# Optimization experiments

Hardware: AMD Instinct MI355X
Metric: run time of the kernel (lower is better)

The kernel has to match this reference:

```python
import jax, jax.numpy as jnp
import numpy as np


def setup_inputs() -> dict:
    key = jax.random.key(0)
    B, E, K = 1024, 1024, 64
    k0, k1, k2, k3, k4, k5 = jax.random.split(key, 6)
    s = 1.0 / np.sqrt(E)  # PyTorch GRU init bound
    c = jax.random.normal(k0, (B, E), dtype=jnp.float32)
    x = jax.random.normal(k1, (B, E, K), dtype=jnp.float32)
    W_ih = jax.random.uniform(k2, (3 * E, E), minval=-s, maxval=s, dtype=jnp.float32)
    W_hh = jax.random.uniform(k3, (3 * E, E), minval=-s, maxval=s, dtype=jnp.float32)
    b_ih = jax.random.uniform(k4, (3 * E,), minval=-s, maxval=s, dtype=jnp.float32)
    b_hh = jax.random.uniform(k5, (3 * E,), minval=-s, maxval=s, dtype=jnp.float32)
    return {"c": c, "x": x, "W_ih": W_ih, "W_hh": W_hh, "b_ih": b_ih, "b_hh": b_hh, "K": K}


def reference(c, x, W_ih, W_hh, b_ih, b_hh, K):
    # c: (B, E) initial hidden state; x: (B, E, T) teacher-forcing sequence.
    # Inputs actually consumed by the GRU: zeros at step 0, then x columns
    # [T-K .. T-2] at steps 1..K-1 (the torch slice at the last step is empty
    # and never used).
    B, E = c.shape
    T = x.shape[2]
    x_t = jnp.transpose(x, (2, 0, 1))  # (T, B, E)
    xs = jnp.concatenate(
        [jnp.zeros((1, B, E), dtype=x.dtype), x_t[T - K : T - 1]], axis=0
    )  # (K, B, E)

    def step(h, xk):
        gi = xk @ W_ih.T + b_ih  # (B, 3E)
        gh = h @ W_hh.T + b_hh   # (B, 3E)
        i_r, i_z, i_n = jnp.split(gi, 3, axis=-1)
        h_r, h_z, h_n = jnp.split(gh, 3, axis=-1)
        r = jax.nn.sigmoid(i_r + h_r)
        z = jax.nn.sigmoid(i_z + h_z)
        n = jnp.tanh(i_n + r * h_n)
        h_new = (1.0 - z) * n + z * h
        return h_new, h_new

    _, ys = jax.lax.scan(step, c, xs)  # ys: (K, B, E)
    y = jnp.transpose(ys, (1, 0, 2))   # (B, K, E) == torch.cat(y_out, dim=1)
    return jnp.transpose(y, (0, 2, 1))  # teacher-forcing transpose -> (B, E, K)
```

## Files before the change

### kernel.cpp

```cpp
#include <hip/hip_runtime.h>
#include <hip/hip_bf16.h>
#include <math.h>

typedef __bf16 bf16x8 __attribute__((ext_vector_type(8)));
typedef float f32x4 __attribute__((ext_vector_type(4)));
typedef unsigned short u16x8 __attribute__((ext_vector_type(8)));

#define VMW(N) asm volatile("s_waitcnt vmcnt(" #N ")" ::: "memory")
#define LGKM0  asm volatile("s_waitcnt lgkmcnt(0)" ::: "memory")
#define CFENCE asm volatile("" ::: "memory")

__device__ inline unsigned short f2b(float f) {
  union { float f; unsigned u; } v; v.f = f;
  unsigned u = v.u;
  return (unsigned short)((u + 0x7fffu + ((u >> 16) & 1u)) >> 16);
}
__device__ inline float b2f(unsigned short s) {
  union { unsigned u; float f; } v; v.u = ((unsigned)s) << 16;
  return v.f;
}
__device__ inline float sigm(float x) { return 1.f / (1.f + __expf(-x)); }
__device__ inline float tanh_f(float x) {
  float e = __expf(2.f * x);
  return 1.f - 2.f / (e + 1.f);
}
__device__ inline void gll16(const unsigned short* g, unsigned short* l) {
  __builtin_amdgcn_global_load_lds(
      (const __attribute__((address_space(1))) void*)g,
      (__attribute__((address_space(3))) void*)l, 16, 0, 0);
}
__device__ inline void gll16u(const unsigned short* g, unsigned short* l) {
  __builtin_amdgcn_global_load_lds(
      (const __attribute__((address_space(1))) void*)g,
      (__attribute__((address_space(3))) void*)l, 16, 0, 17);
}
__device__ inline void as64(unsigned short* p, unsigned long long v) {
  __hip_atomic_store((unsigned long long*)p, v, __ATOMIC_RELAXED,
                     __HIP_MEMORY_SCOPE_AGENT);
}

__global__ __launch_bounds__(256) void prep_kernel(
    const float* __restrict__ Wih, const float* __restrict__ Whh,
    const float* __restrict__ c, unsigned short* __restrict__ Wihb,
    unsigned short* __restrict__ Whhb, unsigned short* __restrict__ hbf,
    float* __restrict__ h32, long nW, long nH)
{
  long stride = (long)gridDim.x * blockDim.x;
  long t0 = (long)blockIdx.x * blockDim.x + threadIdx.x;
  for (long i = t0; i < nW; i += stride) {
    Wihb[i] = f2b(Wih[i]);
    Whhb[i] = f2b(Whh[i]);
  }
  for (long i = t0; i < nH; i += stride) {
    float v = c[i];
    h32[i] = v;
    hbf[i] = f2b(v);
  }
}

__global__ __launch_bounds__(256) void reorder_kernel(
    const unsigned short* __restrict__ Wihb, const unsigned short* __restrict__ Whhb,
    const float* __restrict__ bih, const float* __restrict__ bhh,
    unsigned short* __restrict__ Wihp, unsigned short* __restrict__ Whhp,
    float* __restrict__ bihp, float* __restrict__ bhhp, int E)
{
  int N3 = 3 * E;
  long total = (long)N3 * E;
  long stride = (long)gridDim.x * blockDim.x;
  long t0 = (long)blockIdx.x * blockDim.x + threadIdx.x;
  for (long i = t0; i < total; i += stride) {
    int rp = (int)(i / E);
    int col = (int)(i - (long)rp * E);
    int g6 = rp / 192, rem = rp - g6 * 192;
    int g = rem >> 6, elo = rem & 63;
    long src = ((long)g * E + g6 * 64 + elo) * E + col;
    Wihp[i] = Wihb[src];
    Whhp[i] = Whhb[src];
  }
  for (long i = t0; i < N3; i += stride) {
    int rp = (int)i;
    int g6 = rp / 192, rem = rp - g6 * 192;
    int g = rem >> 6, elo = rem & 63;
    bihp[i] = bih[(long)g * E + g6 * 64 + elo];
    bhhp[i] = bhh[(long)g * E + g6 * 64 + elo];
  }
}

__global__ __launch_bounds__(256) void transpose_x(
    const float* __restrict__ x, unsigned short* __restrict__ XS,
    int B, int E, int K)
{
  __shared__ float T[64][65];
  int e0 = blockIdx.x * 64;
  int b = blockIdx.y;
  int t = threadIdx.x;
  const float* xb = x + ((long)b * E + e0) * K;
#pragma unroll
  for (int i = 0; i < 4; ++i) {
    int cidx = i * 256 + t;
    int e = cidx >> 4;
    int f4 = cidx & 15;
    float4 v = *(const float4*)(xb + (long)e * K + f4 * 4);
    T[e][f4 * 4 + 0] = v.x;
    T[e][f4 * 4 + 1] = v.y;
    T[e][f4 * 4 + 2] = v.z;
    T[e][f4 * 4 + 3] = v.w;
  }
  __syncthreads();
#pragma unroll
  for (int i = 0; i < 16; ++i) {
    int cidx = i * 256 + t;
    int k = cidx >> 6;
    int e = cidx & 63;
    if (k < K - 1)
      XS[((long)(k + 1) * B + b) * E + e0 + e] = f2b(T[e][k]);
  }
}

__global__ __launch_bounds__(512, 1)
void gemm256(const unsigned short* __restrict__ A,
             const unsigned short* __restrict__ Bw,
             const float* __restrict__ bias,
             unsigned short* __restrict__ Cb,
             int M, int N, int K)
{
  __shared__ __align__(16) unsigned short sm[3 * 24576];

  int nwg = gridDim.x * gridDim.y;
  int wg = blockIdx.y * gridDim.x + blockIdx.x;
  if ((nwg & 7) == 0) { int ch = nwg >> 3; wg = (wg & 7) * ch + (wg >> 3); }
  int tx = wg % gridDim.x;
  int ty = wg / gridDim.x;

  const int tid = threadIdx.x;
  const int lane = tid & 63;
  const int wave = tid >> 6;
  const int wm = wave >> 2;
  const int wn = wave & 3;
  const int q = lane >> 4;
  const int l15 = lane & 15;

  const long a_base = (long)ty * 128 * K;
  const long b_base = (long)tx * 256 * K;

  long a_src[2]; int a_dst[2];
#pragma unroll
  for (int i = 0; i < 2; ++i) {
    int c = i * 512 + tid;
    int row = c >> 3;
    int g8 = (c & 7) ^ (row & 7);
    a_src[i] = a_base + (long)row * K + g8 * 8;
    a_dst[i] = c * 8;
  }
  long b_src[4]; int b_dst[4];
#pragma unroll
  for (int i = 0; i < 4; ++i) {
    int c = i * 512 + tid;
    int row = c >> 3;
    int g8 = (c & 7) ^ (row & 7);
    b_src[i] = b_base + (long)row * K + g8 * 8;
    b_dst[i] = c * 8;
  }

  int a_ro[4], b_ro[4];
#pragma unroll
  for (int mi = 0; mi < 4; ++mi) {
    int lr = wm * 64 + mi * 16 + l15;
    a_ro[mi] = lr * 64;
  }
#pragma unroll
  for (int ni = 0; ni < 4; ++ni) {
    int col = wn * 64 + ni * 16 + l15;
    b_ro[ni] = col * 64;
  }

  f32x4 acc[4][4] = {};

  const int NT = K >> 6;
#pragma unroll
  for (int t = 0; t < 2; ++t) {
    unsigned short* As = sm + t * 24576;
    unsigned short* Bs = As + 8192;
#pragma unroll
    for (int i = 0; i < 2; ++i) gll16(A + a_src[i] + t * 64, As + a_dst[i]);
#pragma unroll
    for (int i = 0; i < 4; ++i) gll16(Bw + b_src[i] + t * 64, Bs + b_dst[i]);
  }

  for (int kt = 0; kt < NT; ++kt) {
    if (kt >= NT - 2) VMW(0); else VMW(6);
    __builtin_amdgcn_s_barrier();
    CFENCE;
    const unsigned short* As = sm + (kt % 3) * 24576;
    const unsigned short* Bs = As + 8192;
    unsigned short* As2 = sm + ((kt + 2) % 3) * 24576;
    unsigned short* Bs2 = As2 + 8192;
    const bool st = (kt + 2 < NT);
    const int ko = (kt + 2) * 64;

    if (st) {
      gll16(A + a_src[0] + ko, As2 + a_dst[0]);
      gll16(A + a_src[1] + ko, As2 + a_dst[1]);
      gll16(Bw + b_src[0] + ko, Bs2 + b_dst[0]);
    }
    {
      const int c8 = q;
      bf16x8 af[4], bf_[4];
#pragma unroll
      for (int mi = 0; mi < 4; ++mi) {
        int lr = wm * 64 + mi * 16 + l15;
        af[mi] = *(const bf16x8*)&As[a_ro[mi] + ((c8 ^ (lr & 7)) << 3)];
      }
#pragma unroll
      for (int ni = 0; ni < 4; ++ni) {
        int col = wn * 64 + ni * 16 + l15;
        bf_[ni] = *(const bf16x8*)&Bs[b_ro[ni] + ((c8 ^ (col & 7)) << 3)];
      }
      __builtin_amdgcn_s_setprio(1);
#pragma unroll
      for (int mi = 0; mi < 4; ++mi)
#pragma unroll
        for (int ni = 0; ni < 4; ++ni)
          acc[mi][ni] = __builtin_amdgcn_mfma_f32_16x16x32_bf16(
              af[mi], bf_[ni], acc[mi][ni], 0, 0, 0);
      __builtin_amdgcn_s_setprio(0);
    }
    LGKM0;
    __builtin_amdgcn_s_barrier();
    CFENCE;
    if (st) {
      gll16(Bw + b_src[1] + ko, Bs2 + b_dst[1]);
      gll16(Bw + b_src[2] + ko, Bs2 + b_dst[2]);
      gll16(Bw + b_src[3] + ko, Bs2 + b_dst[3]);
    }
    {
      const int c8 = 4 + q;
      bf16x8 af[4], bf_[4];
#pragma unroll
      for (int mi = 0; mi < 4; ++mi) {
        int lr = wm * 64 + mi * 16 + l15;
        af[mi] = *(const bf16x8*)&As[a_ro[mi] + ((c8 ^ (lr & 7)) << 3)];
      }
#pragma unroll
      for (int ni = 0; ni < 4; ++ni) {
        int col = wn * 64 + ni * 16 + l15;
        bf_[ni] = *(const bf16x8*)&Bs[b_ro[ni] + ((c8 ^ (col & 7)) << 3)];
      }
      __builtin_amdgcn_s_setprio(1);
#pragma unroll
      for (int mi = 0; mi < 4; ++mi)
#pragma unroll
        for (int ni = 0; ni < 4; ++ni)
          acc[mi][ni] = __builtin_amdgcn_mfma_f32_16x16x32_bf16(
              af[mi], bf_[ni], acc[mi][ni], 0, 0, 0);
      __builtin_amdgcn_s_setprio(0);
    }
    LGKM0;
  }

  long crow0 = (long)ty * 128 + wm * 64;
  long ccol0 = (long)tx * 256 + wn * 64;
#pragma unroll
  for (int mi = 0; mi < 4; ++mi) {
#pragma unroll
    for (int ni = 0; ni < 4; ++ni) {
      long col = ccol0 + ni * 16 + l15;
      float bv = bias[col];
#pragma unroll
      for (int j = 0; j < 4; ++j) {
        long row = crow0 + mi * 16 + (q << 2) + j;
        Cb[row * N + col] = f2b(acc[mi][ni][j] + bv);
      }
    }
  }
}

#define BM 128
#define BN 128
#define BKS 64

template<int OUTBF>
__global__ __launch_bounds__(256)
void gemm_bt(const unsigned short* __restrict__ A,
             const unsigned short* __restrict__ Bw,
             const float* __restrict__ bias,
             float* __restrict__ Cf, unsigned short* __restrict__ Cb,
             int M, int N, int K)
{
  __shared__ __align__(16) unsigned short As[BM * BKS];
  __shared__ __align__(16) unsigned short Bs[BN * BKS];

  int nwg = gridDim.x * gridDim.y;
  int wg = blockIdx.y * gridDim.x + blockIdx.x;
  if ((nwg & 7) == 0) { int ch = nwg >> 3; wg = (wg & 7) * ch + (wg >> 3); }
  int tx = wg % gridDim.x;
  int ty = wg / gridDim.x;

  const int tid = threadIdx.x;
  const int lane = tid & 63;
  const int wave = tid >> 6;
  const int wr = wave >> 1, wc = wave & 1;

  f32x4 acc[4][4] = {};

  const long a_base = (long)ty * BM * K;
  const long b_base = (long)tx * BN * K;

  for (int kt = 0; kt < K; kt += BKS) {
    __syncthreads();
#pragma unroll
    for (int i = 0; i < 4; ++i) {
      int c = i * 256 + tid;
      int row = c >> 3, sc = c & 7;
      int gcol8 = sc ^ (row & 7);
      const unsigned short* ga = A + a_base + (long)row * K + kt + gcol8 * 8;
      const unsigned short* gb = Bw + b_base + (long)row * K + kt + gcol8 * 8;
      int cbase = (i * 256 + wave * 64) * 8;
      gll16(ga, &As[cbase]);
      gll16(gb, &Bs[cbase]);
    }
    __syncthreads();
#pragma unroll
    for (int kk = 0; kk < BKS; kk += 32) {
      int kidx = kk + ((lane >> 4) << 3);
      int c8 = kidx >> 3;
      bf16x8 af[4], bfv[4];
#pragma unroll
      for (int m = 0; m < 4; ++m) {
        int row = wr * 64 + m * 16 + (lane & 15);
        af[m] = *(const bf16x8*)&As[row * BKS + ((c8 ^ (row & 7)) << 3)];
      }
#pragma unroll
      for (int n = 0; n < 4; ++n) {
        int col = wc * 64 + n * 16 + (lane & 15);
        bfv[n] = *(const bf16x8*)&Bs[col * BKS + ((c8 ^ (col & 7)) << 3)];
      }
#pragma unroll
      for (int m = 0; m < 4; ++m)
#pragma unroll
        for (int n = 0; n < 4; ++n)
          acc[m][n] = __builtin_amdgcn_mfma_f32_16x16x32_bf16(
              af[m], bfv[n], acc[m][n], 0, 0, 0);
    }
  }

  long crow0 = (long)ty * BM + wr * 64;
  long ccol0 = (long)tx * BN + wc * 64;
#pragma unroll
  for (int m = 0; m < 4; ++m) {
#pragma unroll
    for (int n = 0; n < 4; ++n) {
      long col = ccol0 + n * 16 + (lane & 15);
      float bv = bias[col];
#pragma unroll
      for (int j = 0; j < 4; ++j) {
        long row = crow0 + m * 16 + ((lane >> 4) << 2) + j;
        float v = acc[m][n][j] + bv;
        if (OUTBF) Cb[row * N + col] = f2b(v);
        else       Cf[row * N + col] = v;
      }
    }
  }
}

__global__ __launch_bounds__(512, 1)
void gru_rec4(const unsigned short* __restrict__ GI,
              const unsigned short* __restrict__ Whp,
              const float* __restrict__ bhp,
              const unsigned short* __restrict__ h0,
              unsigned short* __restrict__ hbuf0,
              unsigned short* __restrict__ hbuf1,
              unsigned short* __restrict__ Y,
              unsigned int* __restrict__ bar,
              int B, int E, int K, int net)
{
  __shared__ __align__(16) unsigned char smem[156672];
  unsigned short* Ah  = (unsigned short*)smem;
  unsigned short* Bss = (unsigned short*)(smem + 49152);
  unsigned short* GIs = (unsigned short*)(smem + 122880);
  unsigned short* Ys  = (unsigned short*)(smem + 147456);
  float* Red = (float*)smem;

  const int N3 = 3 * E;
  const int e6 = blockIdx.x;
  const int bt = blockIdx.y;
  const int b0 = bt << 6;
  const int ec0 = e6 * 192;
  const int ecol0 = e6 << 6;
  const int tid = threadIdx.x;
  const int lane = tid & 63;
  const int w = tid >> 6;
  const int ew = w >> 1;
  const int kw = w & 1;
  const int q = lane >> 4;
  const int l15 = lane & 15;
  const int el = (ew << 4) + l15;
  const int c8 = (kw << 2) + q;
  const int axo = (c8 ^ (l15 & 7)) << 3;
  const int bxo = (c8 ^ (el & 7)) << 3;

  const int arow = tid >> 3;
  const int ag8 = (tid & 7) ^ (arow & 7);
  const long a_goff = (long)(b0 + arow) * E + ag8 * 8;
  const int a_dst = tid * 8;
  long b_goff[3]; int b_dst[3];
#pragma unroll
  for (int i = 0; i < 3; ++i) {
    int c = i * 512 + tid;
    int row = c >> 3;
    int g8 = (c & 7) ^ (row & 7);
    b_goff[i] = (long)(ec0 + row) * E + g8 * 8;
    b_dst[i] = c * 8;
  }
  long gi_off[3]; int gi_dst[3];
#pragma unroll
  for (int i = 0; i < 3; ++i) {
    int c = i * 512 + tid;
    int row = c / 24, cc = c - row * 24;
    gi_off[i] = (long)(b0 + row) * N3 + ec0 + cc * 8;
    gi_dst[i] = c * 8;
  }

  const float bh0 = bhp[ec0 + el];
  const float bh1 = bhp[ec0 + 64 + el];
  const float bh2 = bhp[ec0 + 128 + el];

  if (kw == 0) {
#pragma unroll
    for (int m = 0; m < 4; ++m)
#pragma unroll
      for (int j = 0; j < 4; ++j) {
        int row = m * 16 + q * 4 + j;
        Ys[row * 72 + el] = h0[(long)(b0 + row) * E + ecol0 + el];
      }
  }
  __syncthreads();

  for (int k = 0; k < K; ++k) {
    const unsigned short* hprev = (k & 1) ? hbuf1 : hbuf0;
    unsigned short* hnext = (k & 1) ? hbuf0 : hbuf1;
    const unsigned short* GIk = GI + (long)k * B * N3;

#pragma unroll
    for (int i = 0; i < 3; ++i) gll16(GIk + gi_off[i], GIs + gi_dst[i]);
#pragma unroll
    for (int t = 0; t < 5; ++t)
      gll16u(hprev + a_goff + t * 64, Ah + t * 4096 + a_dst);
#pragma unroll
    for (int t = 0; t < 2; ++t)
#pragma unroll
      for (int i = 0; i < 3; ++i)
        gll16(Whp + b_goff[i] + t * 64, Bss + t * 12288 + b_dst[i]);

    f32x4 acc[4][3];
#pragma unroll
    for (int m = 0; m < 4; ++m)
#pragma unroll
      for (int g = 0; g < 3; ++g)
        acc[m][g] = (f32x4){0.f, 0.f, 0.f, 0.f};

#pragma unroll
    for (int kt = 0; kt < 16; ++kt) {
      if (kt == 0)       VMW(3);
      else if (kt == 1)  VMW(4);
      else if (kt <= 11) VMW(5);
      else if (kt == 12) VMW(4);
      else if (kt == 15) VMW(0);
      else               VMW(3);
      LGKM0;
      __builtin_amdgcn_s_barrier();
      CFENCE;

      if (kt + 2 < 16) {
#pragma unroll
        for (int i = 0; i < 3; ++i)
          gll16(Whp + b_goff[i] + (kt + 2) * 64,
                Bss + ((kt + 2) % 3) * 12288 + b_dst[i]);
      }
      if (kt + 5 < 16)
        gll16u(hprev + a_goff + (kt + 5) * 64,
               Ah + ((kt + 5) % 6) * 4096 + a_dst);

      const unsigned short* Ab = Ah + (kt % 6) * 4096;
      const unsigned short* Bb = Bss + (kt % 3) * 12288;
      bf16x8 af[4], bfg[3];
#pragma unroll
      for (int m = 0; m < 4; ++m)
        af[m] = *(const bf16x8*)&Ab[(m * 16 + l15) * 64 + axo];
#pragma unroll
      for (int g = 0; g < 3; ++g)
        bfg[g] = *(const bf16x8*)&Bb[(g * 64 + el) * 64 + bxo];

      __builtin_amdgcn_s_setprio(1);
#pragma unroll
      for (int g = 0; g < 3; ++g)
#pragma unroll
        for (int m = 0; m < 4; ++m)
          acc[m][g] = __builtin_amdgcn_mfma_f32_16x16x32_bf16(
              af[m], bfg[g], acc[m][g], 0, 0, 0);
      __builtin_amdgcn_s_setprio(0);
    }

    __syncthreads();
    float* rp = &Red[((ew << 6) + lane) * 49];
    if (kw == 1) {
#pragma unroll
      for (int m = 0; m < 4; ++m)
#pragma unroll
        for (int g = 0; g < 3; ++g)
#pragma unroll
          for (int cc = 0; cc < 4; ++cc)
            rp[(m * 3 + g) * 4 + cc] = acc[m][g][cc];
    }
    __syncthreads();
    if (kw == 0) {
#pragma unroll
      for (int m = 0; m < 4; ++m) {
#pragma unroll
        for (int j = 0; j < 4; ++j) {
          int row = m * 16 + q * 4 + j;
          float ghr = acc[m][0][j] + rp[(m * 3 + 0) * 4 + j];
          float ghz = acc[m][1][j] + rp[(m * 3 + 1) * 4 + j];
          float ghn = acc[m][2][j] + rp[(m * 3 + 2) * 4 + j];
          float gr = b2f(GIs[row * 192 + el]);
          float gz = b2f(GIs[row * 192 + 64 + el]);
          float gn = b2f(GIs[row * 192 + 128 + el]);
          float hu = b2f(Ys[row * 72 + el]);
          float r = sigm(gr + ghr + bh0);
          float z = sigm(gz + ghz + bh1);
          float n = tanh_f(gn + r * (ghn + bh2));
          float hv = (1.f - z) * n + z * hu;
          Ys[row * 72 + el] = f2b(hv);
        }
      }
    }
    __syncthreads();
    {
      int row = tid >> 3, cc = tid & 7;
      u16x8 v = *(const u16x8*)&Ys[row * 72 + cc * 8];
      unsigned* pv = (unsigned*)&v;
      unsigned long long s0 = ((unsigned long long)pv[1] << 32) | pv[0];
      unsigned long long s1 = ((unsigned long long)pv[3] << 32) | pv[2];
      unsigned short* hp = hnext + (long)(b0 + row) * E + ecol0 + cc * 8;
      as64(hp, s0);
      as64(hp + 4, s1);
      *(u16x8*)(Y + ((long)k * B + b0 + row) * E + ecol0 + cc * 8) = v;
    }
    if (k + 1 < K) {
      __syncthreads();
      if (tid == 0) {
        __hip_atomic_fetch_add(&bar[bt * 64], 1u, __ATOMIC_RELAXED,
                               __HIP_MEMORY_SCOPE_AGENT);
        unsigned target = (unsigned)(k + 1) * (unsigned)net;
        while (__hip_atomic_load(&bar[bt * 64], __ATOMIC_RELAXED,
                                 __HIP_MEMORY_SCOPE_AGENT) < target)
          __builtin_amdgcn_s_sleep(1);
      }
      __syncthreads();
    }
  }
}

template<int YMODE>
__global__ __launch_bounds__(256)
void gru_pointwise(const unsigned short* __restrict__ GIk,
                   const float* __restrict__ gh,
                   float* __restrict__ h, unsigned short* __restrict__ hbf,
                   unsigned short* __restrict__ Yb,
                   float* __restrict__ out, int k, int B, int E, int K)
{
  long i4 = ((long)blockIdx.x * blockDim.x + threadIdx.x) * 4;
  if (i4 >= (long)B * E) return;
  long b = i4 / E;
  long e = i4 - b * E;
  long g0 = b * 3 * E + e;
  ushort4 ir = *(const ushort4*)(GIk + g0);
  ushort4 iz = *(const ushort4*)(GIk + g0 + E);
  ushort4 in4 = *(const ushort4*)(GIk + g0 + 2 * E);
  float4 hr = *(const float4*)(gh + g0);
  float4 hz = *(const float4*)(gh + g0 + E);
  float4 hn = *(const float4*)(gh + g0 + 2 * E);
  float4 hv = *(const float4*)(h + i4);

  float irf[4] = { b2f(ir.x), b2f(ir.y), b2f(ir.z), b2f(ir.w) };
  float izf[4] = { b2f(iz.x), b2f(iz.y), b2f(iz.z), b2f(iz.w) };
  float inf_[4] = { b2f(in4.x), b2f(in4.y), b2f(in4.z), b2f(in4.w) };
  float hrf[4] = { hr.x, hr.y, hr.z, hr.w };
  float hzf[4] = { hz.x, hz.y, hz.z, hz.w };
  float hnf[4] = { hn.x, hn.y, hn.z, hn.w };
  float hvf[4] = { hv.x, hv.y, hv.z, hv.w };
  float hnew[4];
#pragma unroll
  for (int j = 0; j < 4; ++j) {
    float r = sigm(irf[j] + hrf[j]);
    float z = sigm(izf[j] + hzf[j]);
    float n = tanh_f(inf_[j] + r * hnf[j]);
    hnew[j] = (1.f - z) * n + z * hvf[j];
  }
  *(float4*)(h + i4) = make_float4(hnew[0], hnew[1], hnew[2], hnew[3]);
  ushort4 hb = make_ushort4(f2b(hnew[0]), f2b(hnew[1]), f2b(hnew[2]), f2b(hnew[3]));
  *(ushort4*)(hbf + i4) = hb;
  if (YMODE == 1) {
    *(ushort4*)(Yb + ((long)k * B + b) * E + e) = hb;
  } else {
    float* o = out + (b * E + e) * K + k;
    o[0] = hnew[0]; o[K] = hnew[1]; o[2 * K] = hnew[2]; o[3 * K] = hnew[3];
  }
}

__global__ __launch_bounds__(256)
void transpose_y(const unsigned short* __restrict__ Yv, float* __restrict__ out,
                 int B, int E, int K)
{
  __shared__ float T[64][65];
  int e0 = blockIdx.x * 64;
  int b = blockIdx.y;
  int t = threadIdx.x;
#pragma unroll
  for (int i = 0; i < 4; ++i) {
    int c = i * 256 + t;
    int k = c >> 4, f4 = c & 15;
    long off = ((long)k * B + b) * E + e0 + f4 * 4;
    ushort4 v = *(const ushort4*)(Yv + off);
    T[k][f4 * 4 + 0] = b2f(v.x); T[k][f4 * 4 + 1] = b2f(v.y);
    T[k][f4 * 4 + 2] = b2f(v.z); T[k][f4 * 4 + 3] = b2f(v.w);
  }
  __syncthreads();
#pragma unroll
  for (int i = 0; i < 4; ++i) {
    int c = i * 256 + t;
    int e = c >> 4, f4k = c & 15;
    float4 w;
    w.x = T[f4k * 4 + 0][e];
    w.y = T[f4k * 4 + 1][e];
    w.z = T[f4k * 4 + 2][e];
    w.w = T[f4k * 4 + 3][e];
    *(float4*)(out + ((long)b * E + e0 + e) * K + f4k * 4) = w;
  }
}

extern "C" void kernel_launch(void* const* d_in, const int* in_sizes, int n_in,
                              void* d_out, int out_size, void* d_ws, size_t ws_size,
                              hipStream_t stream)
{
  const float* c   = (const float*)d_in[0];
  const float* x   = (const float*)d_in[1];
  const float* Wih = (const float*)d_in[2];
  const float* Whh = (const float*)d_in[3];
  const float* bih = (const float*)d_in[4];
  const float* bhh = (const float*)d_in[5];
  float* out = (float*)d_out;

  long BE = in_sizes[0];
  int E = (int)(sqrtf((float)(in_sizes[2] / 3)) + 0.5f);
  int B = (int)(BE / E);
  int K = (int)(in_sizes[1] / BE);
  int N3 = 3 * E;
  long M_GI = (long)K * B;

  char* w = (char*)d_ws;
  size_t used = 0;
  auto alloc = [&](size_t bytes) -> char* {
    char* p = w + used;
    used += (bytes + 255) & ~(size_t)255;
    return p;
  };
  unsigned short* Wihb  = (unsigned short*)alloc((size_t)N3 * E * 2);
  unsigned short* Whhb  = (unsigned short*)alloc((size_t)N3 * E * 2);
  unsigned short* hb0   = (unsigned short*)alloc((size_t)B * E * 2);
  float* h32            = (float*)alloc((size_t)B * E * 4);
  float* gh             = (float*)alloc((size_t)B * N3 * 4);
  unsigned short* GIstep= (unsigned short*)alloc((size_t)B * N3 * 2);
  unsigned short* XS    = (unsigned short*)alloc((size_t)K * B * E * 2);

  size_t rem = (ws_size > used) ? ws_size - used : 0;
  size_t szW   = (((size_t)N3 * E * 2) + 255) & ~(size_t)255;
  size_t szB3  = (((size_t)N3 * 4) + 255) & ~(size_t)255;
  size_t szHb1 = (((size_t)B * E * 2) + 255) & ~(size_t)255;
  size_t szGI  = (((size_t)K * B * N3 * 2) + 255) & ~(size_t)255;
  size_t szY   = (((size_t)K * B * E * 2) + 255) & ~(size_t)255;
  int nbt = B / 64, net = E / 64;
  size_t szBar = ((size_t)nbt * 64 * 4 + 255) & ~(size_t)255;

  bool canFused = (B == 1024) && (E == 1024) &&
                  (rem >= 2 * szW + 2 * szB3 + szHb1 + szGI + szY + szBar);

  long nW = (long)N3 * E;
  prep_kernel<<<dim3(2048), dim3(256), 0, stream>>>(Wih, Whh, c, Wihb, Whhb,
                                                    hb0, h32, nW, BE);
  hipMemsetAsync(XS, 0, (size_t)B * E * 2, stream);
  transpose_x<<<dim3(E / 64, B), dim3(256), 0, stream>>>(x, XS, B, E, K);

  if (canFused) {
    unsigned short* Wihp = (unsigned short*)alloc(szW);
    unsigned short* Whhp = (unsigned short*)alloc(szW);
    float* bihp          = (float*)alloc(szB3);
    float* bhhp          = (float*)alloc(szB3);
    unsigned short* hb1  = (unsigned short*)alloc(szHb1);
    unsigned short* GI   = (unsigned short*)alloc(szGI);
    unsigned short* Yb   = (unsigned short*)alloc(szY);
    unsigned int*   bar  = (unsigned int*)alloc(szBar);

    reorder_kernel<<<dim3(2048), dim3(256), 0, stream>>>(
        Wihb, Whhb, bih, bhh, Wihp, Whhp, bihp, bhhp, E);

    gemm256<<<dim3(N3 / 256, (int)(M_GI / 128)), dim3(512), 0, stream>>>(
        XS, Wihp, bihp, GI, (int)M_GI, N3, E);
    hipMemsetAsync(bar, 0, szBar, stream);

    const unsigned short* GIc = GI;
    const unsigned short* Whhc = Whhp;
    const float* bhhc = bhhp;
    const unsigned short* h0c = hb0;
    void* args[] = { (void*)&GIc, (void*)&Whhc, (void*)&bhhc, (void*)&h0c,
                     (void*)&hb0, (void*)&hb1, (void*)&Yb,
                     (void*)&bar, (void*)&B, (void*)&E, (void*)&K, (void*)&net };
    hipError_t ce = hipLaunchCooperativeKernel(
        (const void*)gru_rec4, dim3(net, nbt), dim3(512), args, 0, stream);
    if (ce != hipSuccess) {
      (void)hipGetLastError();
      gru_rec4<<<dim3(net, nbt), dim3(512), 0, stream>>>(
          GIc, Whhc, bhhc, h0c, hb0, hb1, Yb, bar, B, E, K, net);
    }
    transpose_y<<<dim3(E / 64, B), dim3(256), 0, stream>>>(Yb, out, B, E, K);
    return;
  }

  int haveY = rem >= szY;
  unsigned short* Yb = haveY ? (unsigned short*)alloc(szY) : nullptr;
  int pgrid = (int)((BE / 4 + 255) / 256);
  for (int k = 0; k < K; ++k) {
    gemm_bt<1><<<dim3(N3 / BN, B / BM), dim3(256), 0, stream>>>(
        XS + (size_t)k * B * E, Wihb, bih, nullptr, GIstep, B, N3, E);
    gemm_bt<0><<<dim3(N3 / BN, B / BM), dim3(256), 0, stream>>>(
        hb0, Whhb, bhh, gh, nullptr, B, N3, E);
    if (haveY)
      gru_pointwise<1><<<dim3(pgrid), dim3(256), 0, stream>>>(
          GIstep, gh, h32, hb0, Yb, out, k, B, E, K);
    else
      gru_pointwise<2><<<dim3(pgrid), dim3(256), 0, stream>>>(
          GIstep, gh, h32, hb0, nullptr, out, k, B, E, K);
  }
  if (haveY)
    transpose_y<<<dim3(E / 64, B), dim3(256), 0, stream>>>(Yb, out, B, E, K);
}
```

Before: 1.480 ms.

## Use 256x256 tile with K=32 stages for input GEMM and fuse weight prep

```diff
diff --git a/kernel.cpp b/kernel.cpp
--- a/kernel.cpp
+++ b/kernel.cpp
@@ -58,11 +58,13 @@
   }
 }
 
-__global__ __launch_bounds__(256) void reorder_kernel(
-    const unsigned short* __restrict__ Wihb, const unsigned short* __restrict__ Whhb,
-    const float* __restrict__ bih, const float* __restrict__ bhh,
+__global__ __launch_bounds__(256) void prep2_kernel(
+    const float* __restrict__ Wih, const float* __restrict__ Whh,
+    const float* __restrict__ c, const float* __restrict__ bih,
+    const float* __restrict__ bhh,
     unsigned short* __restrict__ Wihp, unsigned short* __restrict__ Whhp,
-    float* __restrict__ bihp, float* __restrict__ bhhp, int E)
+    float* __restrict__ bihp, float* __restrict__ bhhp,
+    unsigned short* __restrict__ hb0, int E, long nH)
 {
   int N3 = 3 * E;
   long total = (long)N3 * E;
@@ -74,8 +76,8 @@
     int g6 = rp / 192, rem = rp - g6 * 192;
     int g = rem >> 6, elo = rem & 63;
     long src = ((long)g * E + g6 * 64 + elo) * E + col;
-    Wihp[i] = Wihb[src];
-    Whhp[i] = Whhb[src];
+    Wihp[i] = f2b(Wih[src]);
+    Whhp[i] = f2b(Whh[src]);
   }
   for (long i = t0; i < N3; i += stride) {
     int rp = (int)i;
@@ -84,7 +86,10 @@
     bihp[i] = bih[(long)g * E + g6 * 64 + elo];
     bhhp[i] = bhh[(long)g * E + g6 * 64 + elo];
   }
-}
+  for (long i = t0; i < nH; i += stride)
+    hb0[i] = f2b(c[i]);
+}
+
 
 __global__ __launch_bounds__(256) void transpose_x(
     const float* __restrict__ x, unsigned short* __restrict__ XS,
@@ -118,13 +123,13 @@
 }
 
 __global__ __launch_bounds__(512, 1)
-void gemm256(const unsigned short* __restrict__ A,
-             const unsigned short* __restrict__ Bw,
-             const float* __restrict__ bias,
-             unsigned short* __restrict__ Cb,
-             int M, int N, int K)
-{
-  __shared__ __align__(16) unsigned short sm[3 * 24576];
+void gemm256k32(const unsigned short* __restrict__ A,
+                const unsigned short* __restrict__ Bw,
+                const float* __restrict__ bias,
+                unsigned short* __restrict__ Cb,
+                int M, int N, int K)
+{
+  __shared__ __align__(16) unsigned short sm[3][16384];
 
   int nwg = gridDim.x * gridDim.y;
   int wg = blockIdx.y * gridDim.x + blockIdx.x;
@@ -140,111 +145,65 @@
   const int q = lane >> 4;
   const int l15 = lane & 15;
 
-  const long a_base = (long)ty * 128 * K;
+  const long a_base = (long)ty * 256 * K;
   const long b_base = (long)tx * 256 * K;
 
-  long a_src[2]; int a_dst[2];
+  long ab_off[2]; int dstc[2];
 #pragma unroll
   for (int i = 0; i < 2; ++i) {
     int c = i * 512 + tid;
-    int row = c >> 3;
-    int g8 = (c & 7) ^ (row & 7);
-    a_src[i] = a_base + (long)row * K + g8 * 8;
-    a_dst[i] = c * 8;
-  }
-  long b_src[4]; int b_dst[4];
-#pragma unroll
-  for (int i = 0; i < 4; ++i) {
-    int c = i * 512 + tid;
-    int row = c >> 3;
-    int g8 = (c & 7) ^ (row & 7);
-    b_src[i] = b_base + (long)row * K + g8 * 8;
-    b_dst[i] = c * 8;
-  }
-
-  int a_ro[4], b_ro[4];
-#pragma unroll
-  for (int mi = 0; mi < 4; ++mi) {
-    int lr = wm * 64 + mi * 16 + l15;
-    a_ro[mi] = lr * 64;
-  }
-#pragma unroll
-  for (int ni = 0; ni < 4; ++ni) {
-    int col = wn * 64 + ni * 16 + l15;
-    b_ro[ni] = col * 64;
-  }
-
-  f32x4 acc[4][4] = {};
-
-  const int NT = K >> 6;
+    int row = c >> 2;
+    int g4 = (c & 3) ^ (row & 3);
+    ab_off[i] = (long)row * K + g4 * 8;
+    dstc[i] = c * 8;
+  }
+
+  int arow[8], bcol[4];
+#pragma unroll
+  for (int mi = 0; mi < 8; ++mi) arow[mi] = wm * 128 + mi * 16 + l15;
+#pragma unroll
+  for (int ni = 0; ni < 4; ++ni) bcol[ni] = wn * 64 + ni * 16 + l15;
+
+  f32x4 acc[8][4] = {};
+
+  const int NT = K >> 5;
 #pragma unroll
   for (int t = 0; t < 2; ++t) {
-    unsigned short* As = sm + t * 24576;
-    unsigned short* Bs = As + 8192;
-#pragma unroll
-    for (int i = 0; i < 2; ++i) gll16(A + a_src[i] + t * 64, As + a_dst[i]);
-#pragma unroll
-    for (int i = 0; i < 4; ++i) gll16(Bw + b_src[i] + t * 64, Bs + b_dst[i]);
-  }
-
-  for (int kt = 0; kt < NT; ++kt) {
-    if (kt >= NT - 2) VMW(0); else VMW(6);
-    __builtin_amdgcn_s_barrier();
-    CFENCE;
-    const unsigned short* As = sm + (kt % 3) * 24576;
-    const unsigned short* Bs = As + 8192;
-    unsigned short* As2 = sm + ((kt + 2) % 3) * 24576;
-    unsigned short* Bs2 = As2 + 8192;
-    const bool st = (kt + 2 < NT);
-    const int ko = (kt + 2) * 64;
-
-    if (st) {
-      gll16(A + a_src[0] + ko, As2 + a_dst[0]);
-      gll16(A + a_src[1] + ko, As2 + a_dst[1]);
-      gll16(Bw + b_src[0] + ko, Bs2 + b_dst[0]);
-    }
-    {
-      const int c8 = q;
-      bf16x8 af[4], bf_[4];
-#pragma unroll
-      for (int mi = 0; mi < 4; ++mi) {
-        int lr = wm * 64 + mi * 16 + l15;
-        af[mi] = *(const bf16x8*)&As[a_ro[mi] + ((c8 ^ (lr & 7)) << 3)];
-      }
-#pragma unroll
-      for (int ni = 0; ni < 4; ++ni) {
-        int col = wn * 64 + ni * 16 + l15;
-        bf_[ni] = *(const bf16x8*)&Bs[b_ro[ni] + ((c8 ^ (col & 7)) << 3)];
-      }
-      __builtin_amdgcn_s_setprio(1);
-#pragma unroll
-      for (int mi = 0; mi < 4; ++mi)
-#pragma unroll
-        for (int ni = 0; ni < 4; ++ni)
-          acc[mi][ni] = __builtin_amdgcn_mfma_f32_16x16x32_bf16(
-              af[mi], bf_[ni], acc[mi][ni], 0, 0, 0);
-      __builtin_amdgcn_s_setprio(0);
-    }
-    LGKM0;
+#pragma unroll
+    for (int i = 0; i < 2; ++i)
+      gll16(A + a_base + ab_off[i] + t * 32, &sm[t][dstc[i]]);
+#pragma unroll
+    for (int i = 0; i < 2; ++i)
+      gll16(Bw + b_base + ab_off[i] + t * 32, &sm[t][8192 + dstc[i]]);
+  }
+
+  for (int t = 0; t < NT; ++t) {
+    const int rs = t % 3;
+    const int ws = (t + 2) % 3;
+    const bool st = (t + 2 < NT);
+    const unsigned short* As = sm[rs];
+    const unsigned short* Bs = sm[rs] + 8192;
+
+    if (t == NT - 1) VMW(0); else VMW(4);
     __builtin_amdgcn_s_barrier();
     CFENCE;
     if (st) {
-      gll16(Bw + b_src[1] + ko, Bs2 + b_dst[1]);
-      gll16(Bw + b_src[2] + ko, Bs2 + b_dst[2]);
-      gll16(Bw + b_src[3] + ko, Bs2 + b_dst[3]);
+#pragma unroll
+      for (int i = 0; i < 2; ++i)
+        gll16(A + a_base + ab_off[i] + (t + 2) * 32, &sm[ws][dstc[i]]);
+    }
+    bf16x8 bf[4];
+#pragma unroll
+    for (int ni = 0; ni < 4; ++ni) {
+      int r = bcol[ni];
+      bf[ni] = *(const bf16x8*)&Bs[r * 32 + ((q ^ (r & 3)) << 3)];
     }
     {
-      const int c8 = 4 + q;
-      bf16x8 af[4], bf_[4];
+      bf16x8 af[4];
 #pragma unroll
       for (int mi = 0; mi < 4; ++mi) {
-        int lr = wm * 64 + mi * 16 + l15;
-        af[mi] = *(const bf16x8*)&As[a_ro[mi] + ((c8 ^ (lr & 7)) << 3)];
-      }
-#pragma unroll
-      for (int ni = 0; ni < 4; ++ni) {
-        int col = wn * 64 + ni * 16 + l15;
-        bf_[ni] = *(const bf16x8*)&Bs[b_ro[ni] + ((c8 ^ (col & 7)) << 3)];
+        int r = arow[mi];
+        af[mi] = *(const bf16x8*)&As[r * 32 + ((q ^ (r & 3)) << 3)];
       }
       __builtin_amdgcn_s_setprio(1);
 #pragma unroll
@@ -252,16 +211,38 @@
 #pragma unroll
         for (int ni = 0; ni < 4; ++ni)
           acc[mi][ni] = __builtin_amdgcn_mfma_f32_16x16x32_bf16(
-              af[mi], bf_[ni], acc[mi][ni], 0, 0, 0);
+              af[mi], bf[ni], acc[mi][ni], 0, 0, 0);
       __builtin_amdgcn_s_setprio(0);
     }
-    LGKM0;
-  }
-
-  long crow0 = (long)ty * 128 + wm * 64;
+    __builtin_amdgcn_s_barrier();
+    CFENCE;
+    if (st) {
+#pragma unroll
+      for (int i = 0; i < 2; ++i)
+        gll16(Bw + b_base + ab_off[i] + (t + 2) * 32, &sm[ws][8192 + dstc[i]]);
+    }
+    {
+      bf16x8 af[4];
+#pragma unroll
+      for (int mi = 0; mi < 4; ++mi) {
+        int r = arow[4 + mi];
+        af[mi] = *(const bf16x8*)&As[r * 32 + ((q ^ (r & 3)) << 3)];
+      }
+      __builtin_amdgcn_s_setprio(1);
+#pragma unroll
+      for (int mi = 0; mi < 4; ++mi)
+#pragma unroll
+        for (int ni = 0; ni < 4; ++ni)
+          acc[4 + mi][ni] = __builtin_amdgcn_mfma_f32_16x16x32_bf16(
+              af[mi], bf[ni], acc[4 + mi][ni], 0, 0, 0);
+      __builtin_amdgcn_s_setprio(0);
+    }
+  }
+
+  long crow0 = (long)ty * 256 + wm * 128;
   long ccol0 = (long)tx * 256 + wn * 64;
 #pragma unroll
-  for (int mi = 0; mi < 4; ++mi) {
+  for (int mi = 0; mi < 8; ++mi) {
 #pragma unroll
     for (int ni = 0; ni < 4; ++ni) {
       long col = ccol0 + ni * 16 + l15;
@@ -665,46 +646,37 @@
     used += (bytes + 255) & ~(size_t)255;
     return p;
   };
-  unsigned short* Wihb  = (unsigned short*)alloc((size_t)N3 * E * 2);
-  unsigned short* Whhb  = (unsigned short*)alloc((size_t)N3 * E * 2);
-  unsigned short* hb0   = (unsigned short*)alloc((size_t)B * E * 2);
-  float* h32            = (float*)alloc((size_t)B * E * 4);
-  float* gh             = (float*)alloc((size_t)B * N3 * 4);
-  unsigned short* GIstep= (unsigned short*)alloc((size_t)B * N3 * 2);
-  unsigned short* XS    = (unsigned short*)alloc((size_t)K * B * E * 2);
-
-  size_t rem = (ws_size > used) ? ws_size - used : 0;
+  unsigned short* XS = (unsigned short*)alloc((size_t)K * B * E * 2);
+
   size_t szW   = (((size_t)N3 * E * 2) + 255) & ~(size_t)255;
   size_t szB3  = (((size_t)N3 * 4) + 255) & ~(size_t)255;
-  size_t szHb1 = (((size_t)B * E * 2) + 255) & ~(size_t)255;
+  size_t szHb  = (((size_t)B * E * 2) + 255) & ~(size_t)255;
   size_t szGI  = (((size_t)K * B * N3 * 2) + 255) & ~(size_t)255;
   size_t szY   = (((size_t)K * B * E * 2) + 255) & ~(size_t)255;
   int nbt = B / 64, net = E / 64;
   size_t szBar = ((size_t)nbt * 64 * 4 + 255) & ~(size_t)255;
 
-  bool canFused = (B == 1024) && (E == 1024) &&
-                  (rem >= 2 * szW + 2 * szB3 + szHb1 + szGI + szY + szBar);
-
-  long nW = (long)N3 * E;
-  prep_kernel<<<dim3(2048), dim3(256), 0, stream>>>(Wih, Whh, c, Wihb, Whhb,
-                                                    hb0, h32, nW, BE);
-  hipMemsetAsync(XS, 0, (size_t)B * E * 2, stream);
-  transpose_x<<<dim3(E / 64, B), dim3(256), 0, stream>>>(x, XS, B, E, K);
+  size_t needFused = 2 * szW + 2 * szB3 + 2 * szHb + szGI + szY + szBar;
+  bool canFused = (B == 1024) && (E == 1024) && (K == 64) &&
+                  (ws_size > used) && ((ws_size - used) >= needFused);
 
   if (canFused) {
     unsigned short* Wihp = (unsigned short*)alloc(szW);
     unsigned short* Whhp = (unsigned short*)alloc(szW);
     float* bihp          = (float*)alloc(szB3);
     float* bhhp          = (float*)alloc(szB3);
-    unsigned short* hb1  = (unsigned short*)alloc(szHb1);
+    unsigned short* hb0  = (unsigned short*)alloc(szHb);
+    unsigned short* hb1  = (unsigned short*)alloc(szHb);
     unsigned short* GI   = (unsigned short*)alloc(szGI);
     unsigned short* Yb   = (unsigned short*)alloc(szY);
     unsigned int*   bar  = (unsigned int*)alloc(szBar);
 
-    reorder_kernel<<<dim3(2048), dim3(256), 0, stream>>>(
-        Wihb, Whhb, bih, bhh, Wihp, Whhp, bihp, bhhp, E);
-
-    gemm256<<<dim3(N3 / 256, (int)(M_GI / 128)), dim3(512), 0, stream>>>(
+    prep2_kernel<<<dim3(2048), dim3(256), 0, stream>>>(
+        Wih, Whh, c, bih, bhh, Wihp, Whhp, bihp, bhhp, hb0, E, BE);
+    hipMemsetAsync(XS, 0, (size_t)B * E * 2, stream);
+    transpose_x<<<dim3(E / 64, B), dim3(256), 0, stream>>>(x, XS, B, E, K);
+
+    gemm256k32<<<dim3(N3 / 256, (int)(M_GI / 256)), dim3(512), 0, stream>>>(
         XS, Wihp, bihp, GI, (int)M_GI, N3, E);
     hipMemsetAsync(bar, 0, szBar, stream);
 
@@ -726,8 +698,22 @@
     return;
   }
 
+  unsigned short* Wihb  = (unsigned short*)alloc(szW);
+  unsigned short* Whhb  = (unsigned short*)alloc(szW);
+  unsigned short* hb0   = (unsigned short*)alloc(szHb);
+  float* h32            = (float*)alloc((size_t)B * E * 4);
+  float* gh             = (float*)alloc((size_t)B * N3 * 4);
+  unsigned short* GIstep= (unsigned short*)alloc((size_t)B * N3 * 2);
+  size_t rem = (ws_size > used) ? ws_size - used : 0;
   int haveY = rem >= szY;
   unsigned short* Yb = haveY ? (unsigned short*)alloc(szY) : nullptr;
+
+  long nW = (long)N3 * E;
+  prep_kernel<<<dim3(2048), dim3(256), 0, stream>>>(Wih, Whh, c, Wihb, Whhb,
+                                                    hb0, h32, nW, BE);
+  hipMemsetAsync(XS, 0, (size_t)B * E * 2, stream);
+  transpose_x<<<dim3(E / 64, B), dim3(256), 0, stream>>>(x, XS, B, E, K);
+
   int pgrid = (int)((BE / 4 + 255) / 256);
   for (int k = 0; k < K; ++k) {
     gemm_bt<1><<<dim3(N3 / BN, B / BM), dim3(256), 0, stream>>>(
```

After: 1.446 ms. -2.3%, faster.
